# Optimization experiments

Measured on AMD Instinct MI355X. Metric: run time of the kernel, lower is better.

The kernel has to match this reference:

```python
import jax, jax.numpy as jnp
import numpy as np

N = 50000        # nodes
E = 1600000      # edges (avg degree 32)
D = 64           # emb_dim
H = 2            # heads
NEG_SLOPE = 0.2
BOND_VOCAB = 5   # vocab per bond feature (3 categorical features)


def setup_inputs() -> dict:
    key = jax.random.key(0)
    ks = jax.random.split(key, 8)
    x = jax.random.normal(ks[0], (N, D), jnp.float32)
    edge_index = jax.random.randint(ks[1], (2, E), 0, N)
    edge_attr = jax.random.randint(ks[2], (E, 3), 0, BOND_VOCAB)
    W = jax.random.normal(ks[3], (D, H * D), jnp.float32) / np.float32(np.sqrt(D))
    b_W = jnp.zeros((H * D,), jnp.float32)
    att = jax.random.normal(ks[4], (1, H, 2 * D), jnp.float32) * 0.1
    bias = jnp.zeros((D,), jnp.float32)
    bond_emb = jax.random.normal(ks[5], (3, BOND_VOCAB, H * D), jnp.float32) * 0.1
    return dict(x=x, edge_index=edge_index, edge_attr=edge_attr,
                W=W, b_W=b_W, att=att, bias=bias, bond_emb=bond_emb)


def reference(x, edge_index, edge_attr, W, b_W, att, bias, bond_emb):
    row, col = edge_index[0], edge_index[1]  # src (x_j), dst (x_i / aggregation target)
    # BondEncoder: sum of per-feature categorical embeddings -> [E, H*D]
    e = (bond_emb[0][edge_attr[:, 0]]
         + bond_emb[1][edge_attr[:, 1]]
         + bond_emb[2][edge_attr[:, 2]])
    h = x @ W + b_W                                   # [N, H*D]
    x_j = h[row].reshape(-1, H, D) + e.reshape(-1, H, D)   # message source + edge emb
    x_i = h[col].reshape(-1, H, D)                         # message target
    # attention logits: [E, H]
    alpha = (jnp.concatenate([x_i, x_j], axis=-1) * att).sum(-1)
    alpha = jnp.where(alpha >= 0, alpha, NEG_SLOPE * alpha)  # leaky_relu
    # segment softmax over edge_index[0] (source node), PyG semantics
    m = jax.ops.segment_max(alpha, row, num_segments=N)      # [N, H]
    m = jnp.where(jnp.isfinite(m), m, 0.0)                   # empty segments -> 0
    ea = jnp.exp(alpha - m[row])
    s = jax.ops.segment_sum(ea, row, num_segments=N)
    alpha = ea / (s[row] + 1e-16)
    # weighted messages, scatter-add to destination nodes
    msg = x_j * alpha[:, :, None]                            # [E, H, D]
    aggr = jax.ops.segment_sum(msg, col, num_segments=N)     # [N, H, D]
    # update: mean over heads + bias
    return aggr.mean(axis=1) + bias
```

## Files before the change

### kernel.cpp

```cpp
#include <hip/hip_runtime.h>
#include <hip/hip_bf16.h>
#include <math.h>

#define NEG_SLOPE 0.2f
#define CHUNK 2048
#define NPB2 128
#define SCAP 5120

__device__ __forceinline__ unsigned f2bf(float f) {
  unsigned u = __float_as_uint(f);
  return (u + 0x7fffu + ((u >> 16) & 1u)) >> 16;
}

__global__ __launch_bounds__(256) void k1_gemm(
    const float* __restrict__ x, const float* __restrict__ W,
    const float* __restrict__ bW, const float* __restrict__ att,
    unsigned int* __restrict__ hb, float* __restrict__ ai,
    float* __restrict__ aj, int Nn) {
  int t = threadIdx.x;
  int lane = t & 63;
  int wid = blockIdx.x * (blockDim.x >> 6) + (t >> 6);
  int nwaves = gridDim.x * (blockDim.x >> 6);

  float Wr0[64], Wr1[64];
#pragma unroll
  for (int k = 0; k < 64; ++k) {
    Wr0[k] = W[k * 128 + lane];
    Wr1[k] = W[k * 128 + 64 + lane];
  }
  float bs0 = bW[lane], bs1 = bW[64 + lane];
  float ati0 = att[lane];
  float atj0 = att[64 + lane];
  float ati1 = att[128 + lane];
  float atj1 = att[192 + lane];

  for (int row = wid; row < Nn; row += nwaves) {
    int r = __builtin_amdgcn_readfirstlane(row);
    const float* __restrict__ xr = x + (size_t)r * 64;
    float a0a = 0.f, a0b = 0.f, a1a = 0.f, a1b = 0.f;
#pragma unroll
    for (int k = 0; k < 64; k += 2) {
      float xk0 = xr[k], xk1 = xr[k + 1];
      a0a = fmaf(xk0, Wr0[k], a0a);
      a1a = fmaf(xk0, Wr1[k], a1a);
      a0b = fmaf(xk1, Wr0[k + 1], a0b);
      a1b = fmaf(xk1, Wr1[k + 1], a1b);
    }
    float h0 = a0a + a0b + bs0;
    float h1 = a1a + a1b + bs1;
    hb[(size_t)r * 64 + lane] = f2bf(h0) | (f2bf(h1) << 16);

    float ti0 = ati0 * h0, tj0 = atj0 * h0;
    float ti1 = ati1 * h1, tj1 = atj1 * h1;
    ti0 += __shfl_xor(ti0, 32, 64);
    tj0 += __shfl_xor(tj0, 32, 64);
    ti1 += __shfl_xor(ti1, 32, 64);
    tj1 += __shfl_xor(tj1, 32, 64);
    float mi = (lane < 32) ? ti0 : ti1;
    float mj = (lane < 32) ? tj0 : tj1;
#pragma unroll
    for (int off = 16; off > 0; off >>= 1) {
      mi += __shfl_xor(mi, off, 64);
      mj += __shfl_xor(mj, off, 64);
    }
    if ((lane & 31) == 0) {
      ai[r * 2 + (lane >> 5)] = mi;
      aj[r * 2 + (lane >> 5)] = mj;
    }
  }
}

__global__ __launch_bounds__(256) void k_bin(
    const int* __restrict__ ei, const int* __restrict__ eattr,
    unsigned int* __restrict__ rec, int* __restrict__ cnt_tbl,
    int* __restrict__ base_tbl, unsigned int* __restrict__ rec_src,
    int* __restrict__ cnt_tbl2, int* __restrict__ base_tbl2, int Ee, int NCB) {
  __shared__ unsigned sbuf[CHUNK];
  __shared__ unsigned sbuf2[CHUNK];
  __shared__ int hist[512], cur[512], hist2[512], cur2[512];
  int t = threadIdx.x;
  for (int i = t; i < NCB; i += 256) { hist[i] = 0; hist2[i] = 0; }
  __syncthreads();
  int start = blockIdx.x * CHUNK;
  int end = min(start + CHUNK, Ee);
  int cnt = end - start;
  int cbv[CHUNK / 256], cb2v[CHUNK / 256];
  unsigned pkv[CHUNK / 256], pk2v[CHUNK / 256];
  int nk = 0;
  for (int e = start + t; e < end; e += 256, ++nk) {
    int dst = __builtin_nontemporal_load(&ei[Ee + e]);
    int src = __builtin_nontemporal_load(&ei[e]);
    int a0 = __builtin_nontemporal_load(&eattr[e * 3]);
    int a1 = __builtin_nontemporal_load(&eattr[e * 3 + 1]);
    int a2 = __builtin_nontemporal_load(&eattr[e * 3 + 2]);
    unsigned c012 = (unsigned)(a0 + 5 * a1 + 25 * a2);
    cbv[nk] = dst >> 7;
    pkv[nk] = (unsigned)src | (c012 << 16) | ((unsigned)(dst & 127) << 23);
    cb2v[nk] = src >> 7;
    pk2v[nk] = (unsigned)dst | ((unsigned)(src & 127) << 17) | (c012 << 24);
    atomicAdd(&hist[dst >> 7], 1);
    atomicAdd(&hist2[src >> 7], 1);
  }
  __syncthreads();
  if (t == 0) {
    int s = 0;
    for (int i = 0; i < NCB; ++i) { cur[i] = s; s += hist[i]; }
  }
  if (t == 64) {
    int s = 0;
    for (int i = 0; i < NCB; ++i) { cur2[i] = s; s += hist2[i]; }
  }
  __syncthreads();
  for (int i = t; i < NCB; i += 256) {
    cnt_tbl[blockIdx.x * NCB + i] = hist[i];
    base_tbl[blockIdx.x * NCB + i] = cur[i];
    cnt_tbl2[blockIdx.x * NCB + i] = hist2[i];
    base_tbl2[blockIdx.x * NCB + i] = cur2[i];
  }
  __syncthreads();
  for (int k = 0; k < nk; ++k) {
    int pos = atomicAdd(&cur[cbv[k]], 1);
    sbuf[pos] = pkv[k];
    int pos2 = atomicAdd(&cur2[cb2v[k]], 1);
    sbuf2[pos2] = pk2v[k];
  }
  __syncthreads();
  for (int i = t; i < cnt; i += 256) {
    __builtin_nontemporal_store(sbuf[i], &rec[start + i]);
    __builtin_nontemporal_store(sbuf2[i], &rec_src[start + i]);
  }
}

__global__ __launch_bounds__(256) void k_segoff_a(
    const int* __restrict__ cnt_tbl, int* __restrict__ segdst,
    int* __restrict__ btot, int NCB, int NBLK) {
  __shared__ int s[256];
  int t = threadIdx.x, cb = blockIdx.x;
  int per = (NBLK + 255) / 256;
  int loc[8];
  int sum = 0;
  for (int j = 0; j < per; ++j) {
    int blk = t * per + j;
    int v = (blk < NBLK) ? cnt_tbl[blk * NCB + cb] : 0;
    loc[j] = sum;
    sum += v;
  }
  s[t] = sum;
  __syncthreads();
#pragma unroll
  for (int o = 1; o < 256; o <<= 1) {
    int xv = (t >= o) ? s[t - o] : 0;
    __syncthreads();
    s[t] += xv;
    __syncthreads();
  }
  int excl = s[t] - sum;
  for (int j = 0; j < per; ++j) {
    int blk = t * per + j;
    if (blk < NBLK) segdst[cb * NBLK + blk] = excl + loc[j];
  }
  if (t == 255) btot[cb] = s[255];
}

__global__ __launch_bounds__(512) void k_segoff_b(
    const int* __restrict__ btot, int* __restrict__ coarse_base, int NCB, int Ee) {
  __shared__ int s[512];
  int t = threadIdx.x;
  int v = (t < NCB) ? btot[t] : 0;
  s[t] = v;
  __syncthreads();
#pragma unroll
  for (int o = 1; o < 512; o <<= 1) {
    int xv = (t >= o) ? s[t - o] : 0;
    __syncthreads();
    s[t] += xv;
    __syncthreads();
  }
  if (t < NCB) coarse_base[t] = s[t] - v;
  if (t == 0) coarse_base[NCB] = Ee;
}

__global__ __launch_bounds__(256) void k_sacc(
    const unsigned int* __restrict__ rec_src, const int* __restrict__ cnt_tbl2,
    const int* __restrict__ base_tbl2, const int* __restrict__ segdst2,
    const int* __restrict__ btot2, const float2* __restrict__ ai2,
    const float2* __restrict__ aj2, const float* __restrict__ att,
    const float* __restrict__ bemb, float* __restrict__ sden,
    int Nn, int NCB, int NBLK) {
  __shared__ unsigned ubuf[SCAP];
  __shared__ float sdl[NPB2 * 2];
  __shared__ float2 ajs[NPB2];
  __shared__ float tbl[30];
  int t = threadIdx.x;
  int cb = blockIdx.x;
  if (t < 30) {
    int f = t / 10, rem = t % 10, c = rem >> 1, hh = rem & 1;
    float sacc = 0.f;
    for (int d = 0; d < 64; ++d)
      sacc += att[hh * 128 + 64 + d] * bemb[(f * 5 + c) * 128 + hh * 64 + d];
    tbl[t] = sacc;
  }
  int node0 = cb << 7;
  if (t < NPB2 && node0 + t < Nn) ajs[t] = aj2[node0 + t];
  sdl[t] = 0.f;
  int total = btot2[cb];
  __syncthreads();
  bool fits = (total <= SCAP);

#define SACC_BODY(U, AIV)                                                      \
  {                                                                            \
    int sl = ((U) >> 17) & 127;                                                \
    int c012 = ((U) >> 24) & 127;                                              \
    int a0 = c012 % 5, a1 = (c012 / 5) % 5, a2 = c012 / 25;                    \
    float2 ajv = ajs[sl];                                                      \
    float lg0 = AIV.x + ajv.x + tbl[a0 * 2] + tbl[10 + a1 * 2] +               \
                tbl[20 + a2 * 2];                                              \
    float lg1 = AIV.y + ajv.y + tbl[a0 * 2 + 1] + tbl[10 + a1 * 2 + 1] +       \
                tbl[20 + a2 * 2 + 1];                                          \
    lg0 = lg0 >= 0.f ? lg0 : NEG_SLOPE * lg0;                                  \
    lg1 = lg1 >= 0.f ? lg1 : NEG_SLOPE * lg1;                                  \
    atomicAdd(&sdl[sl * 2], __expf(lg0));                                      \
    atomicAdd(&sdl[sl * 2 + 1], __expf(lg1));                                  \
  }

  if (fits) {
    for (int blk = t; blk < NBLK; blk += 256) {
      int len = cnt_tbl2[blk * NCB + cb];
      if (!len) continue;
      int sp = blk * CHUNK + base_tbl2[blk * NCB + cb];
      int dp = segdst2[cb * NBLK + blk];
      for (int j = 0; j < len; ++j) ubuf[dp + j] = rec_src[sp + j];
    }
    __syncthreads();
    int i = t;
    for (; i + 3 * 256 < total; i += 4 * 256) {
      unsigned u[4];
      float2 aiv[4];
#pragma unroll
      for (int k = 0; k < 4; ++k) u[k] = ubuf[i + k * 256];
#pragma unroll
      for (int k = 0; k < 4; ++k) aiv[k] = ai2[u[k] & 0x1FFFF];
#pragma unroll
      for (int k = 0; k < 4; ++k) SACC_BODY(u[k], aiv[k])
    }
    for (; i < total; i += 256) {
      unsigned u = ubuf[i];
      float2 aiv = ai2[u & 0x1FFFF];
      SACC_BODY(u, aiv)
    }
  } else {
    for (int blk = t; blk < NBLK; blk += 256) {
      int len = cnt_tbl2[blk * NCB + cb];
      int sp = blk * CHUNK + base_tbl2[blk * NCB + cb];
      for (int j = 0; j < len; ++j) {
        unsigned u = rec_src[sp + j];
        float2 aiv = ai2[u & 0x1FFFF];
        SACC_BODY(u, aiv)
      }
    }
  }
#undef SACC_BODY
  __syncthreads();
  if (node0 + (t >> 1) < Nn) sden[(size_t)node0 * 2 + t] = sdl[t];
}

__global__ __launch_bounds__(256) void k_sort(
    const unsigned int* __restrict__ rec, const int* __restrict__ cnt_tbl,
    const int* __restrict__ base_tbl, const int* __restrict__ segdst,
    const int* __restrict__ coarse_base, const float2* __restrict__ ai2,
    const float2* __restrict__ aj2, const float2* __restrict__ sd2,
    const float* __restrict__ att, const float* __restrict__ bemb,
    unsigned int* __restrict__ eix2, float2* __restrict__ alpha2,
    int* __restrict__ off, int Nn, int NCB, int NBLK, int Ee) {
  __shared__ unsigned ubuf[SCAP];
  __shared__ unsigned ubuf2[SCAP];
  __shared__ int hist[NPB2], basex[NPB2], curx[NPB2];
  __shared__ float tbl[30];
  __shared__ float2 ais[NPB2];
  int t = threadIdx.x;
  int cb = blockIdx.x;
  if (t < 30) {
    int f = t / 10, rem = t % 10, c = rem >> 1, hh = rem & 1;
    float sacc = 0.f;
    for (int d = 0; d < 64; ++d)
      sacc += att[hh * 128 + 64 + d] * bemb[(f * 5 + c) * 128 + hh * 64 + d];
    tbl[t] = sacc;
  }
  int node0 = cb << 7;
  if (t < NPB2) {
    hist[t] = 0;
    if (node0 + t < Nn) ais[t] = ai2[node0 + t];
  }
  int gbase = coarse_base[cb];
  int total = coarse_base[cb + 1] - gbase;
  __syncthreads();
  bool fits = (total <= SCAP);

  if (fits) {
    for (int blk = t; blk < NBLK; blk += 256) {
      int len = cnt_tbl[blk * NCB + cb];
      if (!len) continue;
      int sp = blk * CHUNK + base_tbl[blk * NCB + cb];
      int dp = segdst[cb * NBLK + blk];
      for (int j = 0; j < len; ++j) ubuf[dp + j] = rec[sp + j];
    }
    __syncthreads();
    for (int i = t; i < total; i += 256)
      atomicAdd(&hist[(ubuf[i] >> 23) & 127], 1);
    __syncthreads();
    if (t == 0) {
      int s = 0;
      for (int i = 0; i < NPB2; ++i) { basex[i] = s; s += hist[i]; }
    }
    __syncthreads();
    if (t < NPB2) {
      curx[t] = basex[t];
      if (node0 + t < Nn) off[node0 + t] = gbase + basex[t];
    }
    if (cb == 0 && t == 0) off[Nn] = Ee;
    __syncthreads();
    for (int i = t; i < total; i += 256) {
      unsigned u = ubuf[i];
      int pos = atomicAdd(&curx[(u >> 23) & 127], 1);
      ubuf2[pos] = u;
    }
    __syncthreads();

#define OUT_BODY(I, U, AJV, SDV)                                               \
    {                                                                          \
      int src = (U) & 0xFFFF;                                                  \
      int c012 = ((U) >> 16) & 127;                                            \
      int dl = ((U) >> 23) & 127;                                              \
      int a0 = c012 % 5, a1 = (c012 / 5) % 5, a2 = c012 / 25;                  \
      float2 aiv = ais[dl];                                                    \
      float lg0 = aiv.x + AJV.x + tbl[a0 * 2] + tbl[10 + a1 * 2] +             \
                  tbl[20 + a2 * 2];                                            \
      float lg1 = aiv.y + AJV.y + tbl[a0 * 2 + 1] + tbl[10 + a1 * 2 + 1] +     \
                  tbl[20 + a2 * 2 + 1];                                        \
      lg0 = lg0 >= 0.f ? lg0 : NEG_SLOPE * lg0;                                \
      lg1 = lg1 >= 0.f ? lg1 : NEG_SLOPE * lg1;                                \
      eix2[gbase + (I)] = (unsigned)src | ((unsigned)a0 << 16) |               \
                          ((unsigned)a1 << 19) | ((unsigned)a2 << 22);         \
      alpha2[gbase + (I)] = make_float2(__expf(lg0) / (SDV.x + 1e-16f),        \
                                        __expf(lg1) / (SDV.y + 1e-16f));       \
    }

    int i = t;
    for (; i + 3 * 256 < total; i += 4 * 256) {
      unsigned u[4];
      float2 ajv[4], sdv[4];
#pragma unroll
      for (int k = 0; k < 4; ++k) u[k] = ubuf2[i + k * 256];
#pragma unroll
      for (int k = 0; k < 4; ++k) ajv[k] = aj2[u[k] & 0xFFFF];
#pragma unroll
      for (int k = 0; k < 4; ++k) sdv[k] = sd2[u[k] & 0xFFFF];
#pragma unroll
      for (int k = 0; k < 4; ++k) OUT_BODY(i + k * 256, u[k], ajv[k], sdv[k])
    }
    for (; i < total; i += 256) {
      unsigned u = ubuf2[i];
      float2 ajv = aj2[u & 0xFFFF];
      float2 sdv = sd2[u & 0xFFFF];
      OUT_BODY(i, u, ajv, sdv)
    }
#undef OUT_BODY
  } else {
    for (int blk = t; blk < NBLK; blk += 256) {
      int len = cnt_tbl[blk * NCB + cb];
      int sp = blk * CHUNK + base_tbl[blk * NCB + cb];
      for (int j = 0; j < len; ++j)
        atomicAdd(&hist[(rec[sp + j] >> 23) & 127], 1);
    }
    __syncthreads();
    if (t == 0) {
      int s = 0;
      for (int i = 0; i < NPB2; ++i) { basex[i] = s; s += hist[i]; }
    }
    __syncthreads();
    if (t < NPB2) {
      curx[t] = basex[t];
      if (node0 + t < Nn) off[node0 + t] = gbase + basex[t];
    }
    if (cb == 0 && t == 0) off[Nn] = Ee;
    __syncthreads();
    for (int blk = t; blk < NBLK; blk += 256) {
      int len = cnt_tbl[blk * NCB + cb];
      int sp = blk * CHUNK + base_tbl[blk * NCB + cb];
      for (int j = 0; j < len; ++j) {
        unsigned u = rec[sp + j];
        int src = u & 0xFFFF;
        int c012 = (u >> 16) & 127;
        int dl = (u >> 23) & 127;
        int a0 = c012 % 5, a1 = (c012 / 5) % 5, a2 = c012 / 25;
        float2 aiv = ais[dl];
        float2 ajv = aj2[src];
        float2 sdv = sd2[src];
        float lg0 = aiv.x + ajv.x + tbl[a0 * 2] + tbl[10 + a1 * 2] + tbl[20 + a2 * 2];
        float lg1 = aiv.y + ajv.y + tbl[a0 * 2 + 1] + tbl[10 + a1 * 2 + 1] +
                    tbl[20 + a2 * 2 + 1];
        lg0 = lg0 >= 0.f ? lg0 : NEG_SLOPE * lg0;
        lg1 = lg1 >= 0.f ? lg1 : NEG_SLOPE * lg1;
        int pos = gbase + atomicAdd(&curx[dl], 1);
        eix2[pos] = (unsigned)src | ((unsigned)a0 << 16) | ((unsigned)a1 << 19) |
                    ((unsigned)a2 << 22);
        alpha2[pos] = make_float2(__expf(lg0) / (sdv.x + 1e-16f),
                                  __expf(lg1) / (sdv.y + 1e-16f));
      }
    }
  }
}

__global__ __launch_bounds__(256) void k_gather(
    const unsigned int* __restrict__ eix, const float2* __restrict__ alpha2,
    const int* __restrict__ off, const unsigned int* __restrict__ hb,
    const float* __restrict__ bemb, const float* __restrict__ bias,
    float* __restrict__ out, int Nn) {
  __shared__ float bembs[15 * 128];
  __shared__ float wsm[4][32];
  int t = threadIdx.x;
  for (int i = t; i < 15 * 128; i += 256) bembs[i] = bemb[i];
  __syncthreads();
  int wave = t >> 6, lane = t & 63;
  int n = blockIdx.x * 4 + wave;
  if (n >= Nn) return;
  int p0 = __builtin_amdgcn_readfirstlane(off[n]);
  int p1 = __builtin_amdgcn_readfirstlane(off[n + 1]);
  int myf = lane / 5;
  int myc = lane % 5;
  bool active = lane < 15;
  float w0 = 0.f, w1 = 0.f;
  float acc0 = 0.f, acc1 = 0.f;

#define EDGE_BODY(U, HV, AL)                                                   \
  {                                                                            \
    acc0 = fmaf(AL.x, __uint_as_float((HV) << 16), acc0);                      \
    acc1 = fmaf(AL.y, __uint_as_float((HV) & 0xffff0000u), acc1);              \
    int a0 = ((U) >> 16) & 7, a1 = ((U) >> 19) & 7, a2 = ((U) >> 22) & 7;      \
    int sel = myf == 0 ? a0 : (myf == 1 ? a1 : a2);                            \
    float m = (active && myc == sel) ? 1.0f : 0.0f;                            \
    w0 = fmaf(m, AL.x, w0);                                                    \
    w1 = fmaf(m, AL.y, w1);                                                    \
  }

  int p = p0;
  for (; p + 8 <= p1; p += 8) {
    unsigned u[8], hv[8];
    float2 al[8];
#pragma unroll
    for (int k = 0; k < 8; ++k) u[k] = eix[p + k];
#pragma unroll
    for (int k = 0; k < 8; ++k) al[k] = alpha2[p + k];
#pragma unroll
    for (int k = 0; k < 8; ++k) {
      const unsigned* __restrict__ hrow = hb + ((size_t)(u[k] & 0xFFFFu) << 6);
      hv[k] = hrow[lane];
    }
#pragma unroll
    for (int k = 0; k < 8; ++k) EDGE_BODY(u[k], hv[k], al[k])
  }
  for (; p < p1; ++p) {
    unsigned u0 = eix[p];
    float2 al0 = alpha2[p];
    const unsigned* __restrict__ hrow = hb + ((size_t)(u0 & 0xFFFFu) << 6);
    unsigned hv0 = hrow[lane];
    EDGE_BODY(u0, hv0, al0)
  }
#undef EDGE_BODY

  if (active) {
    wsm[wave][lane * 2] = w0;
    wsm[wave][lane * 2 + 1] = w1;
  }
#pragma unroll
  for (int k = 0; k < 15; ++k) {
    acc0 += wsm[wave][k * 2] * bembs[k * 128 + lane];
    acc1 += wsm[wave][k * 2 + 1] * bembs[k * 128 + 64 + lane];
  }
  out[(size_t)n * 64 + lane] = 0.5f * (acc0 + acc1) + bias[lane];
}

extern "C" void kernel_launch(void* const* d_in, const int* in_sizes, int n_in,
                              void* d_out, int out_size, void* d_ws, size_t ws_size,
                              hipStream_t stream) {
  const float* x    = (const float*)d_in[0];
  const int*   ei   = (const int*)d_in[1];
  const int*   eatt = (const int*)d_in[2];
  const float* W    = (const float*)d_in[3];
  const float* bW   = (const float*)d_in[4];
  const float* att  = (const float*)d_in[5];
  const float* bias = (const float*)d_in[6];
  const float* bemb = (const float*)d_in[7];
  int Nn = in_sizes[0] / 64;
  int Ee = in_sizes[1] / 2;
  int NCB = (Nn + NPB2 - 1) / NPB2;
  int NBLK = (Ee + CHUNK - 1) / CHUNK;

  char* ws = (char*)d_ws;
  ws = (char*)(((uintptr_t)ws + 15) & ~(uintptr_t)15);
  float* aj = (float*)ws;                 ws += (size_t)Nn * 2 * 4;
  float* sden = (float*)ws;               ws += (size_t)Nn * 2 * 4;
  float* ai = (float*)ws;                 ws += (size_t)Nn * 2 * 4;
  unsigned int* hb = (unsigned int*)ws;   ws += (size_t)Nn * 64 * 4;
  unsigned int* rec = (unsigned int*)ws;  ws += (size_t)NBLK * CHUNK * 4;
  unsigned int* rec_src = (unsigned int*)ws; ws += (size_t)NBLK * CHUNK * 4;
  unsigned int* eix2 = (unsigned int*)ws; ws += (size_t)Ee * 4;
  float2* alpha2 = (float2*)ws;           ws += (size_t)Ee * 8;
  int* off = (int*)ws;                    ws += (size_t)(Nn + 1) * 4;
  int* cnt_tbl = (int*)ws;                ws += (size_t)NBLK * NCB * 4;
  int* base_tbl = (int*)ws;               ws += (size_t)NBLK * NCB * 4;
  int* cnt_tbl2 = (int*)ws;               ws += (size_t)NBLK * NCB * 4;
  int* base_tbl2 = (int*)ws;              ws += (size_t)NBLK * NCB * 4;
  int* segdst = (int*)ws;                 ws += (size_t)NCB * NBLK * 4;
  int* segdst2 = (int*)ws;                ws += (size_t)NCB * NBLK * 4;
  int* coarse_base = (int*)ws;            ws += (size_t)(NCB + 1) * 4;
  int* btot = (int*)ws;                   ws += (size_t)NCB * 4;
  int* btot2 = (int*)ws;                  ws += (size_t)NCB * 4;

  k1_gemm<<<1024, 256, 0, stream>>>(x, W, bW, att, hb, ai, aj, Nn);
  k_bin<<<NBLK, 256, 0, stream>>>(ei, eatt, rec, cnt_tbl, base_tbl, rec_src,
                                  cnt_tbl2, base_tbl2, Ee, NCB);
  k_segoff_a<<<NCB, 256, 0, stream>>>(cnt_tbl, segdst, btot, NCB, NBLK);
  k_segoff_a<<<NCB, 256, 0, stream>>>(cnt_tbl2, segdst2, btot2, NCB, NBLK);
  k_segoff_b<<<1, 512, 0, stream>>>(btot, coarse_base, NCB, Ee);
  k_sacc<<<NCB, 256, 0, stream>>>(rec_src, cnt_tbl2, base_tbl2, segdst2, btot2,
                                  (const float2*)ai, (const float2*)aj, att,
                                  bemb, sden, Nn, NCB, NBLK);
  k_sort<<<NCB, 256, 0, stream>>>(rec, cnt_tbl, base_tbl, segdst, coarse_base,
                                  (const float2*)ai, (const float2*)aj,
                                  (const float2*)sden, att, bemb, eix2, alpha2,
                                  off, Nn, NCB, NBLK, Ee);
  k_gather<<<(Nn + 3) / 4, 256, 0, stream>>>(eix2, alpha2, off, hb, bemb, bias,
                                             (float*)d_out, Nn);
}
```

Before: 284.8 us.

## Parallelize bin prefix scan, merge segoff launches, persistent gather loop

```diff
diff --git a/kernel.cpp b/kernel.cpp
--- a/kernel.cpp
+++ b/kernel.cpp
@@ -78,6 +78,7 @@
   __shared__ unsigned sbuf[CHUNK];
   __shared__ unsigned sbuf2[CHUNK];
   __shared__ int hist[512], cur[512], hist2[512], cur2[512];
+  __shared__ int ssc[256];
   int t = threadIdx.x;
   for (int i = t; i < NCB; i += 256) { hist[i] = 0; hist2[i] = 0; }
   __syncthreads();
@@ -102,13 +103,56 @@
     atomicAdd(&hist2[src >> 7], 1);
   }
   __syncthreads();
-  if (t == 0) {
-    int s = 0;
-    for (int i = 0; i < NCB; ++i) { cur[i] = s; s += hist[i]; }
-  }
-  if (t == 64) {
-    int s = 0;
-    for (int i = 0; i < NCB; ++i) { cur2[i] = s; s += hist2[i]; }
+  {
+    int per = (NCB + 255) / 256;
+    int loc[4];
+    int lsum = 0;
+#pragma unroll 2
+    for (int j = 0; j < per; ++j) {
+      int idx = t * per + j;
+      int v = (idx < NCB) ? hist[idx] : 0;
+      loc[j] = lsum;
+      lsum += v;
+    }
+    ssc[t] = lsum;
+    __syncthreads();
+#pragma unroll
+    for (int o = 1; o < 256; o <<= 1) {
+      int xv = (t >= o) ? ssc[t - o] : 0;
+      __syncthreads();
+      ssc[t] += xv;
+      __syncthreads();
+    }
+    int excl = ssc[t] - lsum;
+#pragma unroll 2
+    for (int j = 0; j < per; ++j) {
+      int idx = t * per + j;
+      if (idx < NCB) cur[idx] = excl + loc[j];
+    }
+    __syncthreads();
+    lsum = 0;
+#pragma unroll 2
+    for (int j = 0; j < per; ++j) {
+      int idx = t * per + j;
+      int v = (idx < NCB) ? hist2[idx] : 0;
+      loc[j] = lsum;
+      lsum += v;
+    }
+    ssc[t] = lsum;
+    __syncthreads();
+#pragma unroll
+    for (int o = 1; o < 256; o <<= 1) {
+      int xv = (t >= o) ? ssc[t - o] : 0;
+      __syncthreads();
+      ssc[t] += xv;
+      __syncthreads();
+    }
+    excl = ssc[t] - lsum;
+#pragma unroll 2
+    for (int j = 0; j < per; ++j) {
+      int idx = t * per + j;
+      if (idx < NCB) cur2[idx] = excl + loc[j];
+    }
   }
   __syncthreads();
   for (int i = t; i < NCB; i += 256) {
@@ -131,17 +175,23 @@
   }
 }
 
-__global__ __launch_bounds__(256) void k_segoff_a(
+__global__ __launch_bounds__(256) void k_segoff_ab(
     const int* __restrict__ cnt_tbl, int* __restrict__ segdst,
-    int* __restrict__ btot, int NCB, int NBLK) {
+    int* __restrict__ btot, const int* __restrict__ cnt_tbl2,
+    int* __restrict__ segdst2, int* __restrict__ btot2, int NCB, int NBLK) {
   __shared__ int s[256];
-  int t = threadIdx.x, cb = blockIdx.x;
+  int t = threadIdx.x;
+  int bid = blockIdx.x;
+  const int* __restrict__ ct = (bid < NCB) ? cnt_tbl : cnt_tbl2;
+  int* __restrict__ sd = (bid < NCB) ? segdst : segdst2;
+  int* __restrict__ bt = (bid < NCB) ? btot : btot2;
+  int cb = (bid < NCB) ? bid : bid - NCB;
   int per = (NBLK + 255) / 256;
   int loc[8];
   int sum = 0;
   for (int j = 0; j < per; ++j) {
     int blk = t * per + j;
-    int v = (blk < NBLK) ? cnt_tbl[blk * NCB + cb] : 0;
+    int v = (blk < NBLK) ? ct[blk * NCB + cb] : 0;
     loc[j] = sum;
     sum += v;
   }
@@ -157,9 +207,9 @@
   int excl = s[t] - sum;
   for (int j = 0; j < per; ++j) {
     int blk = t * per + j;
-    if (blk < NBLK) segdst[cb * NBLK + blk] = excl + loc[j];
-  }
-  if (t == 255) btot[cb] = s[255];
+    if (blk < NBLK) sd[cb * NBLK + blk] = excl + loc[j];
+  }
+  if (t == 255) bt[cb] = s[255];
 }
 
 __global__ __launch_bounds__(512) void k_segoff_b(
@@ -422,62 +472,66 @@
   for (int i = t; i < 15 * 128; i += 256) bembs[i] = bemb[i];
   __syncthreads();
   int wave = t >> 6, lane = t & 63;
-  int n = blockIdx.x * 4 + wave;
-  if (n >= Nn) return;
-  int p0 = __builtin_amdgcn_readfirstlane(off[n]);
-  int p1 = __builtin_amdgcn_readfirstlane(off[n + 1]);
   int myf = lane / 5;
   int myc = lane % 5;
   bool active = lane < 15;
-  float w0 = 0.f, w1 = 0.f;
-  float acc0 = 0.f, acc1 = 0.f;
+  int myshift = 16 + 3 * myf;
+  int mycEff = active ? myc : 8;
+  float bi = bias[lane];
+  int stride = gridDim.x * 4;
+
+  for (int n = blockIdx.x * 4 + wave; n < Nn; n += stride) {
+    int p0 = __builtin_amdgcn_readfirstlane(off[n]);
+    int p1 = __builtin_amdgcn_readfirstlane(off[n + 1]);
+    float w0 = 0.f, w1 = 0.f;
+    float acc0 = 0.f, acc1 = 0.f;
 
 #define EDGE_BODY(U, HV, AL)                                                   \
-  {                                                                            \
-    acc0 = fmaf(AL.x, __uint_as_float((HV) << 16), acc0);                      \
-    acc1 = fmaf(AL.y, __uint_as_float((HV) & 0xffff0000u), acc1);              \
-    int a0 = ((U) >> 16) & 7, a1 = ((U) >> 19) & 7, a2 = ((U) >> 22) & 7;      \
-    int sel = myf == 0 ? a0 : (myf == 1 ? a1 : a2);                            \
-    float m = (active && myc == sel) ? 1.0f : 0.0f;                            \
-    w0 = fmaf(m, AL.x, w0);                                                    \
-    w1 = fmaf(m, AL.y, w1);                                                    \
-  }
-
-  int p = p0;
-  for (; p + 8 <= p1; p += 8) {
-    unsigned u[8], hv[8];
-    float2 al[8];
-#pragma unroll
-    for (int k = 0; k < 8; ++k) u[k] = eix[p + k];
-#pragma unroll
-    for (int k = 0; k < 8; ++k) al[k] = alpha2[p + k];
-#pragma unroll
-    for (int k = 0; k < 8; ++k) {
-      const unsigned* __restrict__ hrow = hb + ((size_t)(u[k] & 0xFFFFu) << 6);
-      hv[k] = hrow[lane];
-    }
-#pragma unroll
-    for (int k = 0; k < 8; ++k) EDGE_BODY(u[k], hv[k], al[k])
-  }
-  for (; p < p1; ++p) {
-    unsigned u0 = eix[p];
-    float2 al0 = alpha2[p];
-    const unsigned* __restrict__ hrow = hb + ((size_t)(u0 & 0xFFFFu) << 6);
-    unsigned hv0 = hrow[lane];
-    EDGE_BODY(u0, hv0, al0)
-  }
+    {                                                                          \
+      acc0 = fmaf(AL.x, __uint_as_float((HV) << 16), acc0);                    \
+      acc1 = fmaf(AL.y, __uint_as_float((HV) & 0xffff0000u), acc1);            \
+      int sel = (int)(((U) >> myshift) & 7u);                                  \
+      float m = (sel == mycEff) ? 1.0f : 0.0f;                                 \
+      w0 = fmaf(m, AL.x, w0);                                                  \
+      w1 = fmaf(m, AL.y, w1);                                                  \
+    }
+
+    int p = p0;
+    for (; p + 8 <= p1; p += 8) {
+      unsigned u[8], hv[8];
+      float2 al[8];
+#pragma unroll
+      for (int k = 0; k < 8; ++k) u[k] = eix[p + k];
+#pragma unroll
+      for (int k = 0; k < 8; ++k) al[k] = alpha2[p + k];
+#pragma unroll
+      for (int k = 0; k < 8; ++k) {
+        const unsigned* __restrict__ hrow = hb + ((size_t)(u[k] & 0xFFFFu) << 6);
+        hv[k] = hrow[lane];
+      }
+#pragma unroll
+      for (int k = 0; k < 8; ++k) EDGE_BODY(u[k], hv[k], al[k])
+    }
+    for (; p < p1; ++p) {
+      unsigned u0 = eix[p];
+      float2 al0 = alpha2[p];
+      const unsigned* __restrict__ hrow = hb + ((size_t)(u0 & 0xFFFFu) << 6);
+      unsigned hv0 = hrow[lane];
+      EDGE_BODY(u0, hv0, al0)
+    }
 #undef EDGE_BODY
 
-  if (active) {
-    wsm[wave][lane * 2] = w0;
-    wsm[wave][lane * 2 + 1] = w1;
-  }
-#pragma unroll
-  for (int k = 0; k < 15; ++k) {
-    acc0 += wsm[wave][k * 2] * bembs[k * 128 + lane];
-    acc1 += wsm[wave][k * 2 + 1] * bembs[k * 128 + 64 + lane];
-  }
-  out[(size_t)n * 64 + lane] = 0.5f * (acc0 + acc1) + bias[lane];
+    if (active) {
+      wsm[wave][lane * 2] = w0;
+      wsm[wave][lane * 2 + 1] = w1;
+    }
+#pragma unroll
+    for (int k = 0; k < 15; ++k) {
+      acc0 += wsm[wave][k * 2] * bembs[k * 128 + lane];
+      acc1 += wsm[wave][k * 2 + 1] * bembs[k * 128 + 64 + lane];
+    }
+    out[(size_t)n * 64 + lane] = 0.5f * (acc0 + acc1) + bi;
+  }
 }
 
 extern "C" void kernel_launch(void* const* d_in, const int* in_sizes, int n_in,
@@ -520,8 +574,8 @@
   k1_gemm<<<1024, 256, 0, stream>>>(x, W, bW, att, hb, ai, aj, Nn);
   k_bin<<<NBLK, 256, 0, stream>>>(ei, eatt, rec, cnt_tbl, base_tbl, rec_src,
                                   cnt_tbl2, base_tbl2, Ee, NCB);
-  k_segoff_a<<<NCB, 256, 0, stream>>>(cnt_tbl, segdst, btot, NCB, NBLK);
-  k_segoff_a<<<NCB, 256, 0, stream>>>(cnt_tbl2, segdst2, btot2, NCB, NBLK);
+  k_segoff_ab<<<2 * NCB, 256, 0, stream>>>(cnt_tbl, segdst, btot, cnt_tbl2,
+                                           segdst2, btot2, NCB, NBLK);
   k_segoff_b<<<1, 512, 0, stream>>>(btot, coarse_base, NCB, Ee);
   k_sacc<<<NCB, 256, 0, stream>>>(rec_src, cnt_tbl2, base_tbl2, segdst2, btot2,
                                   (const float2*)ai, (const float2*)aj, att,
@@ -530,6 +584,6 @@
                                   (const float2*)ai, (const float2*)aj,
                                   (const float2*)sden, att, bemb, eix2, alpha2,
                                   off, Nn, NCB, NBLK, Ee);
-  k_gather<<<(Nn + 3) / 4, 256, 0, stream>>>(eix2, alpha2, off, hb, bemb, bias,
-                                             (float*)d_out, Nn);
-}
+  k_gather<<<2048, 256, 0, stream>>>(eix2, alpha2, off, hb, bemb, bias,
+                                     (float*)d_out, Nn);
+}
```

After: 293.2 us. +2.9%, slower.
